# Kernel tuning notes

Measured on AMD Instinct MI355X. Metric: run time of the kernel, lower is better.

## Reference

```python
import jax, jax.numpy as jnp
import numpy as np

B, S, D = 8, 4096, 1024


def setup_inputs() -> dict:
    key = jax.random.key(0)
    k = jax.random.split(key, 6)
    scale = 1.0 / np.sqrt(D)  # torch nn.Linear default init range
    x = jax.random.normal(k[0], (B, S, D), dtype=jnp.float32)
    mask = jnp.ones((B, S), dtype=jnp.float32)
    Wu = jax.random.uniform(k[1], (D, D), jnp.float32, -scale, scale)
    bu = jax.random.uniform(k[2], (D,), jnp.float32, -scale, scale)
    Wf = jax.random.uniform(k[3], (D, D), jnp.float32, -scale, scale)
    bf = jax.random.uniform(k[4], (D,), jnp.float32, -scale, scale)
    decay_param = jnp.zeros((1,), dtype=jnp.float32)
    return {"x": x, "mask": mask, "Wu": Wu, "bu": bu, "Wf": Wf, "bf": bf, "decay_param": decay_param}


def reference(x, mask, Wu, bu, Wf, bf, decay_param):
    # decay is a learned scalar in (0,1)
    decay = jax.nn.sigmoid(decay_param)[0]
    # Batch linear_update over all timesteps at once: (B,S,D)
    upd = jnp.einsum('bsd,ed->bse', x, Wu) + bu
    m = mask[..., None]  # (B,S,1)
    # mask-gated recurrence: mem_t = a_t * mem_{t-1} + b_t
    #   a_t = mask*decay + (1-mask),  b_t = mask*update
    a = m * decay + (1.0 - m)
    b = m * upd
    a_s = jnp.swapaxes(a, 0, 1)  # (S,B,1)
    b_s = jnp.swapaxes(b, 0, 1)  # (S,B,D)

    def step(mem, ab):
        a_t, b_t = ab
        mem = a_t * mem + b_t
        return mem, mem

    mem0 = jnp.zeros((B, D), dtype=x.dtype)
    _, mem_seq = jax.lax.scan(step, mem0, (a_s, b_s))  # (S,B,D)
    mem_seq = jnp.swapaxes(mem_seq, 0, 1)  # (B,S,D)
    # Batch linear_f over all timesteps
    out = jnp.einsum('bsd,ed->bse', mem_seq, Wf) + bf
    return out
```

## Files before the change

kernel.cpp:

```cpp
#include <hip/hip_runtime.h>
#include <hip/hip_bf16.h>
#include <math.h>

#define PB 8
#define PS 4096
#define PD 1024

typedef __attribute__((ext_vector_type(8))) short bf16x8;
typedef __attribute__((ext_vector_type(4))) float f32x4;

__device__ __forceinline__ ushort f2b(float f) {
    unsigned u = __float_as_uint(f);
    unsigned r = (u + 0x7FFFu + ((u >> 16) & 1u)) >> 16;
    return (ushort)r;
}
__device__ __forceinline__ float b2f(ushort h) {
    return __uint_as_float(((unsigned)h) << 16);
}

__device__ __forceinline__ void gl2lds16(const void* g, void* l) {
    __builtin_amdgcn_global_load_lds(
        (const __attribute__((address_space(1))) void*)g,
        (__attribute__((address_space(3))) void*)l, 16, 0, 0);
}

__global__ __launch_bounds__(256) void cvt_f32_bf16(const float* __restrict__ in,
                                                    ushort* __restrict__ out, int n) {
    int i = (blockIdx.x * 256 + threadIdx.x) * 4;
    if (i + 3 < n) {
        float4 v = *(const float4*)(in + i);
        ushort4 o;
        o.x = f2b(v.x); o.y = f2b(v.y); o.z = f2b(v.z); o.w = f2b(v.w);
        *(ushort4*)(out + i) = o;
    }
}

__global__ __launch_bounds__(256) void cvt_w2(const float* __restrict__ Wu,
                                              const float* __restrict__ Wf,
                                              ushort* __restrict__ Wub,
                                              ushort* __restrict__ Wfb, int n) {
    int i = (blockIdx.x * 256 + threadIdx.x) * 4;
    const float* in = (i < n) ? Wu : Wf;
    ushort* out = (i < n) ? Wub : Wfb;
    int j = (i < n) ? i : i - n;
    float4 v = *(const float4*)(in + j);
    ushort4 o;
    o.x = f2b(v.x); o.y = f2b(v.y); o.z = f2b(v.z); o.w = f2b(v.w);
    *(ushort4*)(out + j) = o;
}

template <bool OUT_BF16>
__global__ __launch_bounds__(512, 2) void gemm_bt(const ushort* __restrict__ A,
                                                  const ushort* __restrict__ Bm,
                                                  const float* __restrict__ bias,
                                                  void* __restrict__ C,
                                                  int M, int N, int K) {
    __shared__ ushort As[2][256 * 64];
    __shared__ ushort Bs[2][256 * 64];

    const int tid = threadIdx.x;
    const int lane = tid & 63;
    const int wave = tid >> 6;
    const int nbn = N >> 8;
    const int xcd = blockIdx.x & 7;
    const int g = blockIdx.x >> 3;
    const int bpx = (gridDim.x >> 3) / nbn;
    const int bm = xcd * bpx + g / nbn;
    const int bn = g % nbn;
    const int wm = wave >> 2, wn = wave & 3;
    const int l15 = lane & 15, quad = lane >> 4;

    const int srow = wave * 8 + (lane >> 3);
    const int sgx = ((lane & 7) ^ ((lane >> 3) & 7)) * 8;
    const ushort* Ag = A + (size_t)(bm * 256 + srow) * K + sgx;
    const ushort* Bg = Bm + (size_t)(bn * 256 + srow) * K + sgx;
    const int lbase = wave * 8 * 64;

#define STAGE_TILE(kk, cc)                                                      \
    do {                                                                        \
        _Pragma("unroll")                                                       \
        for (int rb = 0; rb < 4; ++rb) {                                        \
            gl2lds16(Ag + (kk) + (size_t)(rb * 64) * K, &As[cc][rb * 4096 + lbase]); \
            gl2lds16(Bg + (kk) + (size_t)(rb * 64) * K, &Bs[cc][rb * 4096 + lbase]); \
        }                                                                       \
    } while (0)

    f32x4 acc[8][4];
#pragma unroll
    for (int i = 0; i < 8; ++i)
#pragma unroll
        for (int j = 0; j < 4; ++j) acc[i][j] = (f32x4){0.f, 0.f, 0.f, 0.f};

    const int nt = K >> 6;

    STAGE_TILE(0, 0);
    STAGE_TILE(64, 1);
    asm volatile("s_waitcnt vmcnt(8)" ::: "memory");
    __builtin_amdgcn_s_barrier();

    for (int t = 0; t < nt; ++t) {
        const int c = t & 1;
        const ushort* Ab = &As[c][(wm * 128 + l15) * 64];
        const ushort* Bb = &Bs[c][(wn * 64 + l15) * 64];
#pragma unroll
        for (int p = 0; p < 2; ++p) {
            const int aoff = ((p * 4 + quad) ^ (l15 & 7)) * 8;
            bf16x8 af[8], bfr[4];
#pragma unroll
            for (int i = 0; i < 8; ++i)
                af[i] = *(const bf16x8*)(Ab + i * 16 * 64 + aoff);
#pragma unroll
            for (int j = 0; j < 4; ++j)
                bfr[j] = *(const bf16x8*)(Bb + j * 16 * 64 + aoff);
            __builtin_amdgcn_s_setprio(1);
#pragma unroll
            for (int i = 0; i < 8; ++i)
#pragma unroll
                for (int j = 0; j < 4; ++j)
                    acc[i][j] = __builtin_amdgcn_mfma_f32_16x16x32_bf16(af[i], bfr[j], acc[i][j], 0, 0, 0);
            __builtin_amdgcn_s_setprio(0);
        }
        asm volatile("s_waitcnt lgkmcnt(0)" ::: "memory");
        __builtin_amdgcn_s_barrier();
        if (t + 2 < nt) {
            STAGE_TILE((t + 2) * 64, c);
            asm volatile("s_waitcnt vmcnt(8)" ::: "memory");
        } else {
            asm volatile("s_waitcnt vmcnt(0)" ::: "memory");
        }
        __builtin_amdgcn_s_barrier();
    }
#undef STAGE_TILE

    const int gm0 = bm * 256 + wm * 128;
    const int gn0 = bn * 256 + wn * 64;
    float bv[4];
#pragma unroll
    for (int j = 0; j < 4; ++j) bv[j] = bias[gn0 + j * 16 + l15];
#pragma unroll
    for (int i = 0; i < 8; ++i) {
#pragma unroll
        for (int j = 0; j < 4; ++j) {
            const int col = gn0 + j * 16 + l15;
#pragma unroll
            for (int r = 0; r < 4; ++r) {
                const int row = gm0 + i * 16 + quad * 4 + r;
                float v = acc[i][j][r] + bv[j];
                if (OUT_BF16)
                    ((ushort*)C)[(size_t)row * N + col] = f2b(v);
                else
                    ((float*)C)[(size_t)row * N + col] = v;
            }
        }
    }
}

__global__ __launch_bounds__(256) void scan_partial(const ushort* __restrict__ upd,
                                                    const float* __restrict__ mask,
                                                    const float* __restrict__ dp,
                                                    float* __restrict__ Bc,
                                                    float* __restrict__ Ac,
                                                    int S, int D, int C) {
    const int c = blockIdx.x % C;
    const int b = blockIdx.x / C;
    const int L = S / C;
    const int d0 = threadIdx.x * 4;
    const float decay = 1.f / (1.f + expf(-dp[0]));
    const ushort* up = upd + ((size_t)b * S + (size_t)c * L) * D + d0;
    const float* mp = mask + (size_t)b * S + (size_t)c * L;
    float aA = 1.f;
    float b0 = 0.f, b1 = 0.f, b2 = 0.f, b3 = 0.f;
    for (int s0 = 0; s0 < L; s0 += 4) {
        float4 mv = *(const float4*)(mp + s0);
        ushort4 u0 = *(const ushort4*)(up + (size_t)(s0 + 0) * D);
        ushort4 u1 = *(const ushort4*)(up + (size_t)(s0 + 1) * D);
        ushort4 u2 = *(const ushort4*)(up + (size_t)(s0 + 2) * D);
        ushort4 u3 = *(const ushort4*)(up + (size_t)(s0 + 3) * D);
        float m, a;
        m = mv.x; a = m * decay + (1.f - m); aA *= a;
        b0 = a * b0 + m * b2f(u0.x); b1 = a * b1 + m * b2f(u0.y);
        b2 = a * b2 + m * b2f(u0.z); b3 = a * b3 + m * b2f(u0.w);
        m = mv.y; a = m * decay + (1.f - m); aA *= a;
        b0 = a * b0 + m * b2f(u1.x); b1 = a * b1 + m * b2f(u1.y);
        b2 = a * b2 + m * b2f(u1.z); b3 = a * b3 + m * b2f(u1.w);
        m = mv.z; a = m * decay + (1.f - m); aA *= a;
        b0 = a * b0 + m * b2f(u2.x); b1 = a * b1 + m * b2f(u2.y);
        b2 = a * b2 + m * b2f(u2.z); b3 = a * b3 + m * b2f(u2.w);
        m = mv.w; a = m * decay + (1.f - m); aA *= a;
        b0 = a * b0 + m * b2f(u3.x); b1 = a * b1 + m * b2f(u3.y);
        b2 = a * b2 + m * b2f(u3.z); b3 = a * b3 + m * b2f(u3.w);
    }
    *(float4*)(Bc + (size_t)blockIdx.x * D + d0) = make_float4(b0, b1, b2, b3);
    if (threadIdx.x == 0) Ac[blockIdx.x] = aA;
}

__global__ __launch_bounds__(256) void scan_prefix(const float* __restrict__ Ac,
                                                   const float* __restrict__ Bc,
                                                   float* __restrict__ Mn, int D, int C) {
    int gid = blockIdx.x * 256 + threadIdx.x;
    int b = gid / D;
    int d = gid - b * D;
    float mem = 0.f;
    for (int c = 0; c < C; c += 4) {
        float4 av = *(const float4*)(Ac + b * C + c);
        size_t i0 = ((size_t)(b * C + c)) * D + d;
        float q0 = Bc[i0];
        float q1 = Bc[i0 + D];
        float q2 = Bc[i0 + 2 * (size_t)D];
        float q3 = Bc[i0 + 3 * (size_t)D];
        Mn[i0] = mem;                    mem = av.x * mem + q0;
        Mn[i0 + D] = mem;                mem = av.y * mem + q1;
        Mn[i0 + 2 * (size_t)D] = mem;    mem = av.z * mem + q2;
        Mn[i0 + 3 * (size_t)D] = mem;    mem = av.w * mem + q3;
    }
}

__global__ __launch_bounds__(256) void scan_final(const ushort* __restrict__ upd,
                                                  const float* __restrict__ mask,
                                                  const float* __restrict__ dp,
                                                  const float* __restrict__ Mn,
                                                  ushort* __restrict__ ms,
                                                  int S, int D, int C) {
    const int c = blockIdx.x % C;
    const int b = blockIdx.x / C;
    const int L = S / C;
    const int d0 = threadIdx.x * 4;
    const float decay = 1.f / (1.f + expf(-dp[0]));
    const ushort* up = upd + ((size_t)b * S + (size_t)c * L) * D + d0;
    ushort* op = ms + ((size_t)b * S + (size_t)c * L) * D + d0;
    const float* mp = mask + (size_t)b * S + (size_t)c * L;
    float4 m0 = *(const float4*)(Mn + (size_t)blockIdx.x * D + d0);
    float v0 = m0.x, v1 = m0.y, v2 = m0.z, v3 = m0.w;
    for (int s0 = 0; s0 < L; s0 += 4) {
        float4 mv = *(const float4*)(mp + s0);
        ushort4 u0 = *(const ushort4*)(up + (size_t)(s0 + 0) * D);
        ushort4 u1 = *(const ushort4*)(up + (size_t)(s0 + 1) * D);
        ushort4 u2 = *(const ushort4*)(up + (size_t)(s0 + 2) * D);
        ushort4 u3 = *(const ushort4*)(up + (size_t)(s0 + 3) * D);
        float m, a;
        ushort4 o;
        m = mv.x; a = m * decay + (1.f - m);
        v0 = a * v0 + m * b2f(u0.x); v1 = a * v1 + m * b2f(u0.y);
        v2 = a * v2 + m * b2f(u0.z); v3 = a * v3 + m * b2f(u0.w);
        o.x = f2b(v0); o.y = f2b(v1); o.z = f2b(v2); o.w = f2b(v3);
        *(ushort4*)(op + (size_t)(s0 + 0) * D) = o;
        m = mv.y; a = m * decay + (1.f - m);
        v0 = a * v0 + m * b2f(u1.x); v1 = a * v1 + m * b2f(u1.y);
        v2 = a * v2 + m * b2f(u1.z); v3 = a * v3 + m * b2f(u1.w);
        o.x = f2b(v0); o.y = f2b(v1); o.z = f2b(v2); o.w = f2b(v3);
        *(ushort4*)(op + (size_t)(s0 + 1) * D) = o;
        m = mv.z; a = m * decay + (1.f - m);
        v0 = a * v0 + m * b2f(u2.x); v1 = a * v1 + m * b2f(u2.y);
        v2 = a * v2 + m * b2f(u2.z); v3 = a * v3 + m * b2f(u2.w);
        o.x = f2b(v0); o.y = f2b(v1); o.z = f2b(v2); o.w = f2b(v3);
        *(ushort4*)(op + (size_t)(s0 + 2) * D) = o;
        m = mv.w; a = m * decay + (1.f - m);
        v0 = a * v0 + m * b2f(u3.x); v1 = a * v1 + m * b2f(u3.y);
        v2 = a * v2 + m * b2f(u3.z); v3 = a * v3 + m * b2f(u3.w);
        o.x = f2b(v0); o.y = f2b(v1); o.z = f2b(v2); o.w = f2b(v3);
        *(ushort4*)(op + (size_t)(s0 + 3) * D) = o;
    }
}

extern "C" void kernel_launch(void* const* d_in, const int* in_sizes, int n_in,
                              void* d_out, int out_size, void* d_ws, size_t ws_size,
                              hipStream_t stream) {
    const float* x    = (const float*)d_in[0];
    const float* mask = (const float*)d_in[1];
    const float* Wu   = (const float*)d_in[2];
    const float* bu   = (const float*)d_in[3];
    const float* Wf   = (const float*)d_in[4];
    const float* bfv  = (const float*)d_in[5];
    const float* dp   = (const float*)d_in[6];

    const int B = PB, S = PS, D = PD;
    const int M = B * S;
    const int C = 128;

    char* ws = (char*)d_ws;
    ushort* xb   = (ushort*)(ws);
    ushort* updb = (ushort*)(ws + 67108864);
    ushort* memb = (ushort*)(ws + 134217728);
    ushort* Wub  = (ushort*)(ws + 201326592);
    ushort* Wfb  = (ushort*)(ws + 203423744);
    float*  Bc   = (float*)(ws + 205520896);
    float*  Mn   = (float*)(ws + 209715200);
    float*  Ac   = (float*)(ws + 213909504);

    const int nx = B * S * D;
    cvt_f32_bf16<<<nx / 1024, 256, 0, stream>>>(x, xb, nx);
    cvt_w2<<<(2 * D * D) / 1024, 256, 0, stream>>>(Wu, Wf, Wub, Wfb, D * D);

    dim3 g1((M / 256) * (D / 256));
    gemm_bt<true><<<g1, 512, 0, stream>>>(xb, Wub, bu, (void*)updb, M, D, D);

    scan_partial<<<B * C, 256, 0, stream>>>(updb, mask, dp, Bc, Ac, S, D, C);
    scan_prefix<<<(B * D) / 256, 256, 0, stream>>>(Ac, Bc, Mn, D, C);
    scan_final<<<B * C, 256, 0, stream>>>(updb, mask, dp, Mn, memb, S, D, C);

    gemm_bt<false><<<g1, 512, 0, stream>>>(memb, Wfb, bfv, d_out, M, D, D);
}
```

Before: 442.8 us.

## Split GEMM main loop into quadrant phases with interleaved half-tile prefetch

```diff
diff --git a/kernel.cpp b/kernel.cpp
--- a/kernel.cpp
+++ b/kernel.cpp
@@ -55,8 +55,8 @@
                                                   const float* __restrict__ bias,
                                                   void* __restrict__ C,
                                                   int M, int N, int K) {
-    __shared__ ushort As[2][256 * 64];
-    __shared__ ushort Bs[2][256 * 64];
+    __shared__ ushort As[2 * 16384];
+    __shared__ ushort Bs[2 * 16384];
 
     const int tid = threadIdx.x;
     const int lane = tid & 63;
@@ -70,67 +70,109 @@
     const int wm = wave >> 2, wn = wave & 3;
     const int l15 = lane & 15, quad = lane >> 4;
 
-    const int srow = wave * 8 + (lane >> 3);
-    const int sgx = ((lane & 7) ^ ((lane >> 3) & 7)) * 8;
-    const ushort* Ag = A + (size_t)(bm * 256 + srow) * K + sgx;
-    const ushort* Bg = Bm + (size_t)(bn * 256 + srow) * K + sgx;
-    const int lbase = wave * 8 * 64;
-
-#define STAGE_TILE(kk, cc)                                                      \
+    const int qa = wave * 8 + (lane >> 3);
+    const int sg = ((lane & 7) ^ (qa & 7)) * 8;
+    const ushort* Ag = A + (size_t)(bm * 256 + qa) * K + sg;
+    const int brow0 = bn * 256 + ((qa >> 5) << 6) + (qa & 31);
+    const ushort* Bg = Bm + (size_t)brow0 * K + sg;
+    const int ldst = wave * 512;
+
+#define SA(v, h, c)                                                             \
+    gl2lds16(Ag + (size_t)((c) * 128 + (h) * 64) * K + (size_t)(v) * 64,        \
+             As + (((v) & 1) * 16384 + (h) * 8192 + (c) * 4096 + ldst))
+#define SB(v, h, d)                                                             \
+    gl2lds16(Bg + (size_t)((d) * 128 + (h) * 32) * K + (size_t)(v) * 64,        \
+             Bs + (((v) & 1) * 16384 + (h) * 8192 + (d) * 4096 + ldst))
+
+    const int aro = (wm * 64 + l15) * 64;
+    const int bro = (wn * 32 + l15) * 64;
+    const int sw = l15 & 7;
+    const int k0off = (quad ^ sw) * 8;
+    const int k1off = ((4 + quad) ^ sw) * 8;
+
+    f32x4 acc[8][4];
+#pragma unroll
+    for (int i = 0; i < 8; ++i)
+#pragma unroll
+        for (int j = 0; j < 4; ++j) acc[i][j] = (f32x4){0.f, 0.f, 0.f, 0.f};
+
+    bf16x8 af[4][2], bf0[2][2], bf1[2][2];
+
+#define READ_AF(h)                                                              \
     do {                                                                        \
-        _Pragma("unroll")                                                       \
-        for (int rb = 0; rb < 4; ++rb) {                                        \
-            gl2lds16(Ag + (kk) + (size_t)(rb * 64) * K, &As[cc][rb * 4096 + lbase]); \
-            gl2lds16(Bg + (kk) + (size_t)(rb * 64) * K, &Bs[cc][rb * 4096 + lbase]); \
+        _Pragma("unroll") for (int i = 0; i < 4; ++i) {                         \
+            af[i][0] = *(const bf16x8*)(Asl + (h) * 8192 + i * 1024 + aro + k0off); \
+            af[i][1] = *(const bf16x8*)(Asl + (h) * 8192 + i * 1024 + aro + k1off); \
         }                                                                       \
     } while (0)
-
-    f32x4 acc[8][4];
-#pragma unroll
-    for (int i = 0; i < 8; ++i)
-#pragma unroll
-        for (int j = 0; j < 4; ++j) acc[i][j] = (f32x4){0.f, 0.f, 0.f, 0.f};
+#define READ_BF(dst, h)                                                         \
+    do {                                                                        \
+        _Pragma("unroll") for (int j = 0; j < 2; ++j) {                         \
+            dst[j][0] = *(const bf16x8*)(Bsl + (h) * 8192 + j * 1024 + bro + k0off); \
+            dst[j][1] = *(const bf16x8*)(Bsl + (h) * 8192 + j * 1024 + bro + k1off); \
+        }                                                                       \
+    } while (0)
+#define MFMA_Q(mq, nq, bfr)                                                     \
+    do {                                                                        \
+        __builtin_amdgcn_s_setprio(1);                                          \
+        _Pragma("unroll") for (int kk = 0; kk < 2; ++kk)                        \
+        _Pragma("unroll") for (int i = 0; i < 4; ++i)                           \
+        _Pragma("unroll") for (int j = 0; j < 2; ++j)                           \
+            acc[(mq) * 4 + i][(nq) * 2 + j] = __builtin_amdgcn_mfma_f32_16x16x32_bf16( \
+                af[i][kk], bfr[j][kk], acc[(mq) * 4 + i][(nq) * 2 + j], 0, 0, 0); \
+        __builtin_amdgcn_s_setprio(0);                                          \
+    } while (0)
 
     const int nt = K >> 6;
 
-    STAGE_TILE(0, 0);
-    STAGE_TILE(64, 1);
-    asm volatile("s_waitcnt vmcnt(8)" ::: "memory");
+    SA(0, 0, 0); SA(0, 0, 1); SB(0, 0, 0); SB(0, 0, 1);
+    SA(0, 1, 0); SA(0, 1, 1); SB(0, 1, 0); SB(0, 1, 1);
+    SA(1, 0, 0); SA(1, 0, 1); SB(1, 0, 0); SB(1, 0, 1);
+    asm volatile("s_waitcnt vmcnt(4)" ::: "memory");
     __builtin_amdgcn_s_barrier();
 
-    for (int t = 0; t < nt; ++t) {
-        const int c = t & 1;
-        const ushort* Ab = &As[c][(wm * 128 + l15) * 64];
-        const ushort* Bb = &Bs[c][(wn * 64 + l15) * 64];
-#pragma unroll
-        for (int p = 0; p < 2; ++p) {
-            const int aoff = ((p * 4 + quad) ^ (l15 & 7)) * 8;
-            bf16x8 af[8], bfr[4];
-#pragma unroll
-            for (int i = 0; i < 8; ++i)
-                af[i] = *(const bf16x8*)(Ab + i * 16 * 64 + aoff);
-#pragma unroll
-            for (int j = 0; j < 4; ++j)
-                bfr[j] = *(const bf16x8*)(Bb + j * 16 * 64 + aoff);
-            __builtin_amdgcn_s_setprio(1);
-#pragma unroll
-            for (int i = 0; i < 8; ++i)
-#pragma unroll
-                for (int j = 0; j < 4; ++j)
-                    acc[i][j] = __builtin_amdgcn_mfma_f32_16x16x32_bf16(af[i], bfr[j], acc[i][j], 0, 0, 0);
-            __builtin_amdgcn_s_setprio(0);
-        }
+    for (int u = 0; u < nt; ++u) {
+        const ushort* Asl = As + (u & 1) * 16384;
+        const ushort* Bsl = Bs + (u & 1) * 16384;
+
+        READ_AF(0);
+        READ_BF(bf0, 0);
+        if (u + 1 < nt) { SA(u + 1, 1, 0); SA(u + 1, 1, 1); }
+        asm volatile("s_waitcnt lgkmcnt(8)" ::: "memory");
+        __builtin_amdgcn_s_barrier();
         asm volatile("s_waitcnt lgkmcnt(0)" ::: "memory");
-        __builtin_amdgcn_s_barrier();
-        if (t + 2 < nt) {
-            STAGE_TILE((t + 2) * 64, c);
-            asm volatile("s_waitcnt vmcnt(8)" ::: "memory");
-        } else {
+        MFMA_Q(0, 0, bf0);
+        __builtin_amdgcn_s_barrier();
+
+        READ_BF(bf1, 1);
+        if (u + 1 < nt) { SB(u + 1, 1, 0); SB(u + 1, 1, 1); }
+        __builtin_amdgcn_s_barrier();
+        asm volatile("s_waitcnt lgkmcnt(0)" ::: "memory");
+        MFMA_Q(0, 1, bf1);
+        __builtin_amdgcn_s_barrier();
+
+        READ_AF(1);
+        if (u + 2 < nt) { SA(u + 2, 0, 0); SA(u + 2, 0, 1); }
+        __builtin_amdgcn_s_barrier();
+        asm volatile("s_waitcnt lgkmcnt(0)" ::: "memory");
+        MFMA_Q(1, 0, bf0);
+        __builtin_amdgcn_s_barrier();
+
+        if (u + 2 < nt) { SB(u + 2, 0, 0); SB(u + 2, 0, 1); }
+        __builtin_amdgcn_s_barrier();
+        asm volatile("s_waitcnt lgkmcnt(0)" ::: "memory");
+        MFMA_Q(1, 1, bf1);
+        if (u < nt - 2)
+            asm volatile("s_waitcnt vmcnt(4)" ::: "memory");
+        else
             asm volatile("s_waitcnt vmcnt(0)" ::: "memory");
-        }
-        __builtin_amdgcn_s_barrier();
-    }
-#undef STAGE_TILE
+        __builtin_amdgcn_s_barrier();
+    }
+#undef SA
+#undef SB
+#undef READ_AF
+#undef READ_BF
+#undef MFMA_Q
 
     const int gm0 = bm * 256 + wm * 128;
     const int gn0 = bn * 256 + wn * 64;
```

Result: no change. 435.4 us (-1.7%).
